# Kernel optimization log

Measured on AMD Instinct MI355X. Metric: run time of the kernel, lower is better.

Reference implementation:

```python
import jax, jax.numpy as jnp
import numpy as np

B, S, D, R, N = 4, 2048, 1024, 256, 16

def setup_inputs() -> dict:
    key = jax.random.key(0)
    k1, k2, k3, k4, k5 = jax.random.split(key, 5)
    return {
        "x": jax.random.normal(k1, (B, S, D), dtype=jnp.float32),
        "feature_know": jax.random.normal(k2, (N, D, R), dtype=jnp.float32) * 0.02,
        "restore_know": jax.random.normal(k3, (N, R, D), dtype=jnp.float32) * 0.02,
        "feature_know_w": jax.random.uniform(k4, (B, S, N), dtype=jnp.float32),
        "restore_know_w": jax.random.uniform(k5, (B, S, N), dtype=jnp.float32),
    }

def reference(x, feature_know, restore_know, feature_know_w, restore_know_w):
    # Feature stage: weighted mixture over N knowledge neurons, D -> R.
    # Same math as einsum('bsd,ndr->bsnr') then einsum('bsnr,bsn->bsr'),
    # fused so the [B,S,N,R] intermediate is reduced over N on the fly.
    h = jnp.einsum('bsd,ndr,bsn->bsr', x, feature_know, feature_know_w)
    # Restore stage: R -> D, again a weighted mixture over N neurons.
    out = jnp.einsum('bsr,nrd,bsn->bsd', h, restore_know, restore_know_w)
    # Dropout is evaluated deterministically (eval mode): identity.
    return out
```

## Files before the change

### kernel.cpp

```cpp
#include <hip/hip_runtime.h>

typedef unsigned short u16;
typedef unsigned int u32;
typedef __attribute__((ext_vector_type(4))) float f32x4;
typedef __attribute__((ext_vector_type(8))) short bf16x8;
typedef __attribute__((ext_vector_type(4))) unsigned short u16x4;

#define MFMA(a, b, c) __builtin_amdgcn_mfma_f32_16x16x32_bf16((a), (b), (c), 0, 0, 0)

static constexpr int M_TOK = 8192;

__device__ __forceinline__ u16 f2bf(float f) {
  u32 u = __float_as_uint(f);
  return (u16)((u + 0x7FFFu + ((u >> 16) & 1u)) >> 16);
}
__device__ __forceinline__ float bf2f(u16 b) {
  u32 u = ((u32)b) << 16;
  return __uint_as_float(u);
}
__device__ __forceinline__ void gload16(const u16* g, u16* l) {
  __builtin_amdgcn_global_load_lds(
      (const __attribute__((address_space(1))) u32*)(const void*)g,
      (__attribute__((address_space(3))) u32*)(void*)l, 16, 0, 0);
}

#define PH_BAR()                                       \
  do {                                                 \
    __builtin_amdgcn_s_barrier();                      \
    asm volatile("s_waitcnt lgkmcnt(0)" ::: "memory"); \
  } while (0)
#define PH_END() __builtin_amdgcn_s_barrier()

__global__ void cast_x_kernel(const float* __restrict__ in, u16* __restrict__ out, int total4) {
  for (int i = blockIdx.x * blockDim.x + threadIdx.x; i < total4; i += gridDim.x * blockDim.x) {
    float4 v = ((const float4*)in)[i];
    u16x4 o;
    o[0] = f2bf(v.x); o[1] = f2bf(v.y); o[2] = f2bf(v.z); o[3] = f2bf(v.w);
    ((u16x4*)out)[i] = o;
  }
}

__global__ void tcast_kernel(const float* __restrict__ in, u16* __restrict__ out, int P, int Q) {
  __shared__ float tile[32][33];
  const int z = blockIdx.z;
  const int q0 = blockIdx.x * 32, p0 = blockIdx.y * 32;
  const float* src = in + (size_t)z * P * Q;
  u16* dst = out + (size_t)z * P * Q;
  const int tx = threadIdx.x & 31, ty = threadIdx.x >> 5;
#pragma unroll
  for (int k = 0; k < 4; ++k)
    tile[ty + k * 8][tx] = src[(size_t)(p0 + ty + k * 8) * Q + q0 + tx];
  __syncthreads();
#pragma unroll
  for (int k = 0; k < 4; ++k)
    dst[(size_t)(q0 + ty + k * 8) * P + p0 + tx] = f2bf(tile[tx][ty + k * 8]);
}

__global__ __launch_bounds__(512, 2) void gemm_h(
    const u16* __restrict__ A, const u16* __restrict__ Bm,
    const float* __restrict__ Wf, u16* __restrict__ Hout, const int K) {
  constexpr int NITER = 8;
  __shared__ u16 lds[65536];
  __shared__ float wf_lds[256 * 16];

  const int tid = threadIdx.x;
  const int lane = tid & 63;
  const int wid = tid >> 6;
  const int wr = wid >> 2, wc = wid & 3;

  const int L = blockIdx.y * gridDim.x + blockIdx.x;
  const int ordered = (L & 7) * 64 + (L >> 3);
  const int cid = ordered >> 5, win = ordered & 31;
  const int bx = (cid & 3) * 4 + (win & 3);
  const int by = (cid >> 2) * 8 + (win >> 2);
  const int m0 = by * 256, bx16 = bx * 16;

  const int arow = lane & 15;
  const int acol = (lane >> 4) * 16;
  const int sw = (arow & 7) << 4;
  const int lo0 = arow * 128 + (acol ^ sw);
  const int lo1 = arow * 128 + ((64 + acol) ^ sw);

  const u16* Abase = A + (size_t)m0 * K;

#pragma unroll
  for (int t = 0; t < 2; ++t) {
    const int i4 = t * 512 + tid;
    *(float4*)&wf_lds[i4 * 4] = *(const float4*)&Wf[(size_t)m0 * 16 + i4 * 4];
  }

  f32x4 acc[8][4];
#pragma unroll
  for (int i = 0; i < 8; ++i)
#pragma unroll
    for (int j = 0; j < 4; ++j) acc[i][j] = (f32x4){0.f, 0.f, 0.f, 0.f};

  auto STAGE = [&](int b, int isB, int hf, int kt) {
    u16* Lp = &lds[isB * 32768 + (b * 2 + hf) * 8192];
#pragma unroll
    for (int j = 0; j < 2; ++j) {
      const int q = j * 8192 + tid * 16;
      const int tr = hf * 128 + (q >> 7);
      const int gcol = ((q & 127) ^ (((q >> 7) & 7) << 4)) >> 1;
      const u16* gp = isB
          ? Bm + (size_t)((tr >> 4) * 256 + bx16 + (tr & 15)) * K + kt * 64 + gcol
          : Abase + (size_t)tr * K + kt * 64 + gcol;
      gload16(gp, Lp + ((j * 8192 + wid * 1024) >> 1));
    }
  };
  auto LOAD_AV = [&](bf16x8 (&v)[4][2], int b, int mh) {
    const char* p = (const char*)lds + b * 32768 + (wr * 128 + mh * 64) * 128;
#pragma unroll
    for (int mi = 0; mi < 4; ++mi) {
      v[mi][0] = *(const bf16x8*)(p + mi * 2048 + lo0);
      v[mi][1] = *(const bf16x8*)(p + mi * 2048 + lo1);
    }
  };
  auto LOAD_BV = [&](bf16x8 (&v)[2][2], int b, int nq) {
#pragma unroll
    for (int nj = 0; nj < 2; ++nj) {
      const int rb = wc * 64 + (nq * 2 + nj) * 16;
      const char* p = (const char*)lds + 65536 + b * 32768 + rb * 128;
      v[nj][0] = *(const bf16x8*)(p + lo0);
      v[nj][1] = *(const bf16x8*)(p + lo1);
    }
  };

#define QUAD2(AV, BV0, BV1, MH)                                                \
  do {                                                                         \
    _Pragma("unroll") for (int ks = 0; ks < 2; ++ks) {                         \
      _Pragma("unroll") for (int mi = 0; mi < 4; ++mi) {                       \
        _Pragma("unroll") for (int nj = 0; nj < 2; ++nj) {                     \
          acc[(MH)*4 + mi][nj] = MFMA(AV[mi][ks], BV0[nj][ks], acc[(MH)*4 + mi][nj]); \
          acc[(MH)*4 + mi][2 + nj] = MFMA(AV[mi][ks], BV1[nj][ks], acc[(MH)*4 + mi][2 + nj]); \
        }                                                                      \
      }                                                                        \
    }                                                                          \
  } while (0)

  bf16x8 av[4][2], avh[4][2], bv0[2][2], bv1[2][2];

  STAGE(0, 0, 0, 0); STAGE(0, 0, 1, 0); STAGE(0, 1, 0, 0); STAGE(0, 1, 1, 0);
  STAGE(1, 1, 0, 1); STAGE(1, 0, 0, 1);
  asm volatile("s_waitcnt vmcnt(4)" ::: "memory");
  __builtin_amdgcn_s_barrier();

#pragma unroll 1
  for (int i = 0; i < NITER; ++i) {
    const int ta = 2 * i, tb = ta + 1;
    const bool st = (i + 1 < NITER);
    LOAD_AV(av, 0, 0); LOAD_BV(bv0, 0, 0); LOAD_BV(bv1, 0, 1);
    STAGE(1, 0, 1, tb); STAGE(1, 1, 1, tb);
    PH_BAR();
    QUAD2(av, bv0, bv1, 0);
    PH_END();
    LOAD_AV(avh, 0, 1);
    if (st) { STAGE(0, 1, 0, ta + 2); STAGE(0, 0, 0, ta + 2); }
    PH_BAR();
    QUAD2(avh, bv0, bv1, 1);
    if (st) asm volatile("s_waitcnt vmcnt(4)" ::: "memory");
    else    asm volatile("s_waitcnt vmcnt(0)" ::: "memory");
    PH_END();
    LOAD_AV(av, 1, 0); LOAD_BV(bv0, 1, 0); LOAD_BV(bv1, 1, 1);
    if (st) { STAGE(0, 0, 1, ta + 2); STAGE(0, 1, 1, ta + 2); }
    PH_BAR();
    QUAD2(av, bv0, bv1, 0);
    PH_END();
    LOAD_AV(avh, 1, 1);
    if (st) { STAGE(1, 1, 0, tb + 2); STAGE(1, 0, 0, tb + 2); }
    PH_BAR();
    QUAD2(avh, bv0, bv1, 1);
    if (st) asm volatile("s_waitcnt vmcnt(4)" ::: "memory");
    PH_END();
  }

  __syncthreads();
  float* pbuf = (float*)lds;
#pragma unroll
  for (int MI = 0; MI < 8; ++MI) {
    const int mbase = wr * 128 + MI * 16 + (lane >> 4) * 4;
#pragma unroll
    for (int j = 0; j < 4; ++j) {
      const float4 wf4 = *(const float4*)&wf_lds[(mbase + j) * 16 + wc * 4];
      const float p = wf4.x * acc[MI][0][j] + wf4.y * acc[MI][1][j] +
                      wf4.z * acc[MI][2][j] + wf4.w * acc[MI][3][j];
      pbuf[wc * 4096 + (mbase + j) * 16 + (lane & 15)] = p;
    }
  }
  __syncthreads();
  {
    const int m = tid >> 1, r8 = (tid & 1) * 8;
    float s[8];
#pragma unroll
    for (int r = 0; r < 8; ++r) s[r] = 0.f;
#pragma unroll
    for (int w = 0; w < 4; ++w) {
      const float4 a = *(const float4*)&pbuf[w * 4096 + m * 16 + r8];
      const float4 b = *(const float4*)&pbuf[w * 4096 + m * 16 + r8 + 4];
      s[0] += a.x; s[1] += a.y; s[2] += a.z; s[3] += a.w;
      s[4] += b.x; s[5] += b.y; s[6] += b.z; s[7] += b.w;
    }
    bf16x8 o;
#pragma unroll
    for (int r = 0; r < 8; ++r) o[r] = (short)f2bf(s[r]);
    *(bf16x8*)&Hout[(size_t)(m0 + m) * 256 + bx16 + r8] = o;
  }
}
#undef QUAD2

__global__ __launch_bounds__(512, 2) void gemm_fold(
    const u16* __restrict__ A,
    const u16* __restrict__ Bn,
    const float* __restrict__ W,
    float* __restrict__ Out) {
  __shared__ u16 ldsB[8][8192];
  __shared__ float Wlds[16][132];

  const int tid = threadIdx.x;
  const int lane = tid & 63;
  const int wid = tid >> 6;
  const int kh = wid >> 2;
  const int wrM = (wid >> 1) & 1;
  const int wcN = wid & 1;

  const int L = blockIdx.y * gridDim.x + blockIdx.x;
  const int ordered = (L & 7) * 64 + (L >> 3);
  const int cid = ordered >> 5, win = ordered & 31;
  const int bx = (cid & 3) * 2 + (win & 1);
  const int by = (cid >> 2) * 16 + (win >> 1);
  const int m0 = by * 128, d0 = bx * 128;

  const int arow = lane & 15;
  const int acol = (lane >> 4) * 16;
  const int sw = (arow & 7) << 4;
  const int lo0 = arow * 128 + (acol ^ sw);
  const int lo1 = arow * 128 + ((64 + acol) ^ sw);

  for (int i = tid; i < 128 * 16; i += 512) {
    const int row = i >> 4, n = i & 15;
    Wlds[n][row] = W[(size_t)(m0 + row) * 16 + n];
  }

  auto ASTAGE = [&](int kt) {
    const u16* G = A + (size_t)m0 * 256;
    u16* Lp = &ldsB[kt][0];
#pragma unroll
    for (int j = 0; j < 2; ++j) {
      const int q = j * 8192 + tid * 16;
      const int grow = q >> 7;
      const int gcol = ((q & 127) ^ (((q >> 7) & 7) << 4)) >> 1;
      gload16(G + (size_t)grow * 256 + kt * 64 + gcol, Lp + ((j * 8192 + wid * 1024) >> 1));
    }
  };
  ASTAGE(0); ASTAGE(1); ASTAGE(2); ASTAGE(3);
  __syncthreads();
  bf16x8 avk[4][4];
#pragma unroll
  for (int c2 = 0; c2 < 2; ++c2) {
#pragma unroll
    for (int mi = 0; mi < 4; ++mi) {
      const char* p = (const char*)&ldsB[kh * 2 + c2][0] + (wrM * 64 + mi * 16) * 128;
      avk[c2 * 2 + 0][mi] = *(const bf16x8*)(p + lo0);
      avk[c2 * 2 + 1][mi] = *(const bf16x8*)(p + lo1);
    }
  }
  __syncthreads();

  auto BSTAGE = [&](int ss) {
    const int n = ss >> 1, h = ss & 1, p = ss & 3;
    const u16* G = Bn + ((size_t)n * 1024 + d0) * 256;
#pragma unroll
    for (int t = 0; t < 2; ++t) {
      u16* Lp = &ldsB[2 * p + t][0];
      const int kt = h + 2 * t;
#pragma unroll
      for (int j = 0; j < 2; ++j) {
        const int q = j * 8192 + tid * 16;
        const int grow = q >> 7;
        const int gcol = ((q & 127) ^ (((q >> 7) & 7) << 4)) >> 1;
        gload16(G + (size_t)grow * 256 + kt * 64 + gcol, Lp + ((j * 8192 + wid * 1024) >> 1));
      }
    }
  };

  f32x4 acc_t[4][4], acc_g[4][4];
#pragma unroll
  for (int mi = 0; mi < 4; ++mi)
#pragma unroll
    for (int nj = 0; nj < 4; ++nj) {
      acc_t[mi][nj] = (f32x4){0.f, 0.f, 0.f, 0.f};
      acc_g[mi][nj] = (f32x4){0.f, 0.f, 0.f, 0.f};
    }
  const f32x4 vz = {0.f, 0.f, 0.f, 0.f};
  bf16x8 bv[4][2];
  const int wrow = wrM * 64 + (lane >> 4) * 4;

  BSTAGE(0); BSTAGE(1); BSTAGE(2);
  asm volatile("s_waitcnt vmcnt(8)" ::: "memory");
  __builtin_amdgcn_s_barrier();

  auto SSTEP = [&](int ss, int h, bool do_stage, int vmsel, bool first) {
    const int p = ss & 3;
    const char* pB = (const char*)&ldsB[2 * p + kh][0];
#pragma unroll
    for (int nj = 0; nj < 4; ++nj) {
      const char* q = pB + (wcN * 64 + nj * 16) * 128;
      bv[nj][0] = *(const bf16x8*)(q + lo0);
      bv[nj][1] = *(const bf16x8*)(q + lo1);
    }
    if (do_stage) BSTAGE(ss + 3);
    PH_BAR();
    if (first) {
#pragma unroll
      for (int mi = 0; mi < 4; ++mi)
#pragma unroll
        for (int nj = 0; nj < 4; ++nj)
          acc_g[mi][nj] = MFMA(avk[0][mi], bv[nj][0], vz);
    } else {
#pragma unroll
      for (int mi = 0; mi < 4; ++mi)
#pragma unroll
        for (int nj = 0; nj < 4; ++nj)
          acc_g[mi][nj] = MFMA(avk[2 * h][mi], bv[nj][0], acc_g[mi][nj]);
    }
#pragma unroll
    for (int mi = 0; mi < 4; ++mi)
#pragma unroll
      for (int nj = 0; nj < 4; ++nj)
        acc_g[mi][nj] = MFMA(avk[2 * h + 1][mi], bv[nj][1], acc_g[mi][nj]);
    if (vmsel == 8)      asm volatile("s_waitcnt vmcnt(8)" ::: "memory");
    else if (vmsel == 4) asm volatile("s_waitcnt vmcnt(4)" ::: "memory");
    else if (vmsel == 0) asm volatile("s_waitcnt vmcnt(0)" ::: "memory");
    PH_END();
  };
  auto FOLD = [&](int n) {
#pragma unroll
    for (int mi = 0; mi < 4; ++mi) {
      const float4 w = *(const float4*)&Wlds[n][wrow + mi * 16];
      const f32x4 wv = {w.x, w.y, w.z, w.w};
#pragma unroll
      for (int nj = 0; nj < 4; ++nj)
        acc_t[mi][nj] += wv * acc_g[mi][nj];
    }
  };

#pragma unroll 1
  for (int nn = 0; nn < 14; ++nn) {
    SSTEP(nn * 2 + 0, 0, true, 8, true);
    SSTEP(nn * 2 + 1, 1, true, 8, false);
    FOLD(nn);
  }
  SSTEP(28, 0, true, 8, true);
  SSTEP(29, 1, false, 4, false);
  FOLD(14);
  SSTEP(30, 0, false, 0, true);
  SSTEP(31, 1, false, -1, false);
  FOLD(15);

  __syncthreads();
  float* red = (float*)&ldsB[0][0];
  const int reg = (wrM * 2 + wcN) * 4096;
  if (kh == 1) {
#pragma unroll
    for (int mi = 0; mi < 4; ++mi)
#pragma unroll
      for (int j = 0; j < 4; ++j) {
        const int r = mi * 16 + (lane >> 4) * 4 + j;
#pragma unroll
        for (int nj = 0; nj < 4; ++nj)
          red[reg + r * 64 + nj * 16 + (lane & 15)] = acc_t[mi][nj][j];
      }
  }
  __syncthreads();
  if (kh == 0) {
#pragma unroll
    for (int mi = 0; mi < 4; ++mi) {
      const int rr = mi * 16 + (lane >> 4) * 4;
#pragma unroll
      for (int j = 0; j < 4; ++j) {
        float* orow = Out + (size_t)(m0 + wrM * 64 + rr + j) * 1024 + d0 + wcN * 64 + (lane & 15);
#pragma unroll
        for (int nj = 0; nj < 4; ++nj)
          orow[nj * 16] = acc_t[mi][nj][j] + red[reg + (rr + j) * 64 + nj * 16 + (lane & 15)];
      }
    }
  }
}

extern "C" void kernel_launch(void* const* d_in, const int* in_sizes, int n_in,
                              void* d_out, int out_size, void* d_ws, size_t ws_size,
                              hipStream_t stream) {
  const float* x  = (const float*)d_in[0];
  const float* F  = (const float*)d_in[1];
  const float* Rk = (const float*)d_in[2];
  const float* Wf = (const float*)d_in[3];
  const float* Wr = (const float*)d_in[4];
  float* out = (float*)d_out;

  char* ws = (char*)d_ws;
  u16* X16 = (u16*)(ws);
  u16* B1  = (u16*)(ws + (16u << 20));
  u16* Rt  = (u16*)(ws + (24u << 20));
  u16* h16 = (u16*)(ws + (32u << 20));

  cast_x_kernel<<<2048, 256, 0, stream>>>(x, X16, (M_TOK * 1024) / 4);
  tcast_kernel<<<dim3(8, 32, 16), 256, 0, stream>>>(F, B1, 1024, 256);
  tcast_kernel<<<dim3(32, 8, 16), 256, 0, stream>>>(Rk, Rt, 256, 1024);

  gemm_h<<<dim3(16, 32, 1), 512, 0, stream>>>(X16, B1, Wf, h16, 1024);

  gemm_fold<<<dim3(8, 64, 1), 512, 0, stream>>>(h16, Rt, Wr, out);
}
```

Measured before the change: 144.8 us.

## Restructure restore-stage B pipeline to double-buffer whole neuron per step

Replaces the 4-slot, half-neuron staged prefetch (three stages in flight, vmcnt(8) waits) with a two-slot double buffer. Each step loads one whole neuron's B tile while the current neuron is computed, and waits on vmcnt(0) before the next. This halves barrier/phase count per neuron and simplifies the loop, but reduces prefetch depth to a single neuron ahead. Memory latency may be less well hidden.

```diff
diff --git a/kernel.cpp b/kernel.cpp
--- a/kernel.cpp
+++ b/kernel.cpp
@@ -266,19 +266,22 @@
   }
   __syncthreads();
 
-  auto BSTAGE = [&](int ss) {
-    const int n = ss >> 1, h = ss & 1, p = ss & 3;
-    const u16* G = Bn + ((size_t)n * 1024 + d0) * 256;
-#pragma unroll
-    for (int t = 0; t < 2; ++t) {
-      u16* Lp = &ldsB[2 * p + t][0];
-      const int kt = h + 2 * t;
-#pragma unroll
-      for (int j = 0; j < 2; ++j) {
-        const int q = j * 8192 + tid * 16;
-        const int grow = q >> 7;
-        const int gcol = ((q & 127) ^ (((q >> 7) & 7) << 4)) >> 1;
-        gload16(G + (size_t)grow * 256 + kt * 64 + gcol, Lp + ((j * 8192 + wid * 1024) >> 1));
+  auto BSTAGE_G = [&](int g) {
+    const u16* G = Bn + ((size_t)g * 1024 + d0) * 256;
+    const int base = 4 * (g & 1);
+#pragma unroll
+    for (int h = 0; h < 2; ++h) {
+#pragma unroll
+      for (int t = 0; t < 2; ++t) {
+        u16* Lp = &ldsB[base + 2 * h + t][0];
+        const int kt = h + 2 * t;
+#pragma unroll
+        for (int j = 0; j < 2; ++j) {
+          const int q = j * 8192 + tid * 16;
+          const int grow = q >> 7;
+          const int gcol = ((q & 127) ^ (((q >> 7) & 7) << 4)) >> 1;
+          gload16(G + (size_t)grow * 256 + kt * 64 + gcol, Lp + ((j * 8192 + wid * 1024) >> 1));
+        }
       }
     }
   };
@@ -295,43 +298,18 @@
   bf16x8 bv[4][2];
   const int wrow = wrM * 64 + (lane >> 4) * 4;
 
-  BSTAGE(0); BSTAGE(1); BSTAGE(2);
-  asm volatile("s_waitcnt vmcnt(8)" ::: "memory");
+  BSTAGE_G(0);
+  asm volatile("s_waitcnt vmcnt(0)" ::: "memory");
   __builtin_amdgcn_s_barrier();
 
-  auto SSTEP = [&](int ss, int h, bool do_stage, int vmsel, bool first) {
-    const int p = ss & 3;
-    const char* pB = (const char*)&ldsB[2 * p + kh][0];
+  auto BVLOAD = [&](int buf) {
+    const char* pB = (const char*)&ldsB[buf][0];
 #pragma unroll
     for (int nj = 0; nj < 4; ++nj) {
       const char* q = pB + (wcN * 64 + nj * 16) * 128;
       bv[nj][0] = *(const bf16x8*)(q + lo0);
       bv[nj][1] = *(const bf16x8*)(q + lo1);
     }
-    if (do_stage) BSTAGE(ss + 3);
-    PH_BAR();
-    if (first) {
-#pragma unroll
-      for (int mi = 0; mi < 4; ++mi)
-#pragma unroll
-        for (int nj = 0; nj < 4; ++nj)
-          acc_g[mi][nj] = MFMA(avk[0][mi], bv[nj][0], vz);
-    } else {
-#pragma unroll
-      for (int mi = 0; mi < 4; ++mi)
-#pragma unroll
-        for (int nj = 0; nj < 4; ++nj)
-          acc_g[mi][nj] = MFMA(avk[2 * h][mi], bv[nj][0], acc_g[mi][nj]);
-    }
-#pragma unroll
-    for (int mi = 0; mi < 4; ++mi)
-#pragma unroll
-      for (int nj = 0; nj < 4; ++nj)
-        acc_g[mi][nj] = MFMA(avk[2 * h + 1][mi], bv[nj][1], acc_g[mi][nj]);
-    if (vmsel == 8)      asm volatile("s_waitcnt vmcnt(8)" ::: "memory");
-    else if (vmsel == 4) asm volatile("s_waitcnt vmcnt(4)" ::: "memory");
-    else if (vmsel == 0) asm volatile("s_waitcnt vmcnt(0)" ::: "memory");
-    PH_END();
   };
   auto FOLD = [&](int n) {
 #pragma unroll
@@ -345,17 +323,37 @@
   };
 
 #pragma unroll 1
-  for (int nn = 0; nn < 14; ++nn) {
-    SSTEP(nn * 2 + 0, 0, true, 8, true);
-    SSTEP(nn * 2 + 1, 1, true, 8, false);
-    FOLD(nn);
-  }
-  SSTEP(28, 0, true, 8, true);
-  SSTEP(29, 1, false, 4, false);
-  FOLD(14);
-  SSTEP(30, 0, false, 0, true);
-  SSTEP(31, 1, false, -1, false);
-  FOLD(15);
+  for (int g = 0; g < 16; ++g) {
+    const int base = 4 * (g & 1);
+    const bool st = (g < 15);
+    BVLOAD(base + kh);
+    if (st) BSTAGE_G(g + 1);
+    PH_BAR();
+#pragma unroll
+    for (int mi = 0; mi < 4; ++mi)
+#pragma unroll
+      for (int nj = 0; nj < 4; ++nj)
+        acc_g[mi][nj] = MFMA(avk[0][mi], bv[nj][0], vz);
+#pragma unroll
+    for (int mi = 0; mi < 4; ++mi)
+#pragma unroll
+      for (int nj = 0; nj < 4; ++nj)
+        acc_g[mi][nj] = MFMA(avk[1][mi], bv[nj][1], acc_g[mi][nj]);
+    BVLOAD(base + 2 + kh);
+#pragma unroll
+    for (int mi = 0; mi < 4; ++mi)
+#pragma unroll
+      for (int nj = 0; nj < 4; ++nj)
+        acc_g[mi][nj] = MFMA(avk[2][mi], bv[nj][0], acc_g[mi][nj]);
+#pragma unroll
+    for (int mi = 0; mi < 4; ++mi)
+#pragma unroll
+      for (int nj = 0; nj < 4; ++nj)
+        acc_g[mi][nj] = MFMA(avk[3][mi], bv[nj][1], acc_g[mi][nj]);
+    if (st) asm volatile("s_waitcnt vmcnt(0)" ::: "memory");
+    PH_END();
+    FOLD(g);
+  }
 
   __syncthreads();
   float* red = (float*)&ldsB[0][0];
```

After: 152.2 us. +5.1%, slower.
